# Optimization experiments

Hardware: AMD Instinct MI355X
Metric: run time of the kernel (lower is better)

The kernel has to match this reference:

```python
import jax, jax.numpy as jnp
import numpy as np

HEADS = (4, 2, 1)
OUTS = (32, 16, 2)
NEG_SLOPE = 0.2


def gat_conv(x, src, dst, W, att_s, att_d, b, heads, out_dim, n_nodes, concat):
    # x: [N, Fin] -> h: [N, H, Fout]
    h = (x @ W).reshape(n_nodes, heads, out_dim)
    # per-node attention terms, gathered to edges: [E, H]
    a_src = jnp.sum(h * att_s, axis=-1)
    a_dst = jnp.sum(h * att_d, axis=-1)
    logits = jax.nn.leaky_relu(a_src[src] + a_dst[dst], NEG_SLOPE)
    # segment softmax over incoming edges of each destination node
    lmax = jax.ops.segment_max(logits, dst, num_segments=n_nodes)[dst]
    e = jnp.exp(logits - lmax)
    denom = jax.ops.segment_sum(e, dst, num_segments=n_nodes)[dst]
    alpha = e / denom  # [E, H]
    # weighted message aggregation
    msg = h[src] * alpha[:, :, None]  # [E, H, Fout]
    agg = jax.ops.segment_sum(msg, dst, num_segments=n_nodes)  # [N, H, Fout]
    if concat:
        agg = agg.reshape(n_nodes, heads * out_dim)
    else:
        agg = agg.mean(axis=1)
    return agg + b


def _glorot(key, shape):
    fan = shape[0] + shape[-1] if len(shape) == 2 else shape[-1] * 2
    s = jnp.sqrt(6.0 / fan)
    return jax.random.uniform(key, shape, jnp.float32, -s, s)


def setup_inputs() -> dict:
    key = jax.random.key(0)
    N, E, FIN = 100000, 1600000, 128
    ks = jax.random.split(key, 16)
    x = jax.random.normal(ks[0], (N, FIN), jnp.float32)
    edge_index = jax.random.randint(ks[1], (2, E), 0, N, jnp.int64)
    ins = (FIN, HEADS[0] * OUTS[0], HEADS[1] * OUTS[1])
    d = {"x": x, "edge_index": edge_index}
    for i in range(3):
        H, O = HEADS[i], OUTS[i]
        d[f"W{i+1}"] = _glorot(ks[2 + 4 * i], (ins[i], H * O))
        d[f"att_s{i+1}"] = _glorot(ks[3 + 4 * i], (H, O))
        d[f"att_d{i+1}"] = _glorot(ks[4 + 4 * i], (H, O))
        bdim = H * O if i < 2 else O
        d[f"b{i+1}"] = jnp.zeros((bdim,), jnp.float32)
    return d


def reference(x, edge_index, W1, att_s1, att_d1, b1, W2, att_s2, att_d2, b2, W3, att_s3, att_d3, b3):
    N = x.shape[0]
    loops = jnp.arange(N, dtype=edge_index.dtype)
    src = jnp.concatenate([edge_index[0], loops])
    dst = jnp.concatenate([edge_index[1], loops])
    h = gat_conv(x, src, dst, W1, att_s1, att_d1, b1, HEADS[0], OUTS[0], N, True)
    h = jax.nn.elu(h)
    h = gat_conv(h, src, dst, W2, att_s2, att_d2, b2, HEADS[1], OUTS[1], N, True)
    h = jax.nn.elu(h)
    h = gat_conv(h, src, dst, W3, att_s3, att_d3, b3, HEADS[2], OUTS[2], N, False)
    return jax.nn.log_softmax(h, axis=1)
```

## Files before the change

### kernel.cpp

```cpp
#include <hip/hip_runtime.h>
#include <math.h>

static __device__ __forceinline__ float lrelu(float x){ return fmaxf(x, 0.2f*x); }
static __device__ __forceinline__ float eluf(float x){ return x > 0.f ? x : __expf(x)-1.f; }
static __device__ __forceinline__ float fexp2(float x){ return __builtin_amdgcn_exp2f(x); }
static __device__ __forceinline__ unsigned short f2bf(float f){
  unsigned int u = __float_as_uint(f);
  unsigned int r = (u + 0x7FFFu + ((u>>16)&1u)) >> 16;
  return (unsigned short)r;
}
static __device__ __forceinline__ float bflo(unsigned int u){ return __uint_as_float(u<<16); }
static __device__ __forceinline__ float bfhi(unsigned int u){ return __uint_as_float(u & 0xFFFF0000u); }

#define LOG2E 1.44269504f
#define CLAMP2 115.41f
#define ECAP 4096

typedef __attribute__((ext_vector_type(8))) short short8;
typedef __attribute__((ext_vector_type(4))) float f32x4;

static __device__ __forceinline__ uint4 ld16(const uint4* base, unsigned eoff){
  return *(const uint4*)((const char*)base + (size_t)(eoff*16u));
}
static __device__ __forceinline__ float ldf(const float* base, unsigned eoff){
  return *(const float*)((const char*)base + (size_t)(eoff*4u));
}

#define DETECT_IS64(ei_, s_is64_) \
  if (threadIdx.x < 64){ \
    int w_ = ((const int*)(ei_))[2*threadIdx.x + 1]; \
    unsigned long long b_ = __ballot(w_ != 0); \
    if (threadIdx.x == 0) s_is64_ = (b_ == 0ull); \
  } \
  __syncthreads();

__global__ void k_wprep(const float* __restrict__ W1, const float* __restrict__ W2,
                        unsigned short* __restrict__ wf1, unsigned short* __restrict__ wf2,
                        int* __restrict__ gcnt, int NB){
  int e = blockIdx.x*256 + threadIdx.x;
  if (e < NB) gcnt[e] = 0;
  if (e < 2048){
    int lane = e&63, ct = (e>>6)&7, ks = e>>9;
    int q = lane>>4, n = lane&15;
    union { unsigned short us[8]; uint4 u; } pk;
    #pragma unroll
    for (int j=0;j<8;j++)
      pk.us[j] = f2bf(W1[(ks*32 + q*8 + j)*128 + ct*16 + n]);
    *(uint4*)&wf1[(size_t)e*8] = pk.u;
  } else if (e < 2048+512){
    int e2 = e - 2048;
    int lane = e2&63, ct = (e2>>6)&1, ks = e2>>7;
    int q = lane>>4, n = lane&15;
    union { unsigned short us[8]; uint4 u; } pk;
    #pragma unroll
    for (int j=0;j<8;j++)
      pk.us[j] = f2bf(W2[(ks*32 + q*8 + j)*32 + ct*16 + n]);
    *(uint4*)&wf2[(size_t)e2*8] = pk.u;
  }
}

#define BS_ITEMS 16
__global__ __launch_bounds__(256, 4) void k_scat_gemm1(
    const void* __restrict__ ei, int* __restrict__ gcnt,
    unsigned int* __restrict__ ebuf, int E, int NB, int GS,
    const float* __restrict__ x, const unsigned short* __restrict__ wf,
    const float* __restrict__ atts, const float* __restrict__ attd,
    unsigned short* __restrict__ hb, float* __restrict__ as_, float* __restrict__ ad_,
    int N){
  __shared__ __align__(16) unsigned char smem[32768];
  __shared__ int s_is64;
  int t = threadIdx.x;
  if ((int)blockIdx.x < GS){
    int* lcnt  = (int*)smem;
    int* lbase = lcnt + NB;
    for (int i=t; i<NB; i+=256) lcnt[i]=0;
    DETECT_IS64(ei, s_is64)
    bool is64 = s_is64 != 0;
    int base = blockIdx.x*(256*BS_ITEMS);
    unsigned int ent[BS_ITEMS]; int bk[BS_ITEMS]; int lofs[BS_ITEMS];
    #pragma unroll
    for (int i=0;i<BS_ITEMS;i++){
      int e = base + i*256 + t;
      if (e < E){
        int s, d;
        if (is64){ const long long* p=(const long long*)ei; s=(int)p[e]; d=(int)p[(size_t)E+e]; }
        else     { const int* p=(const int*)ei;            s=p[e];      d=p[(size_t)E+e]; }
        int b = d>>7;
        bk[i] = b;
        ent[i] = (unsigned int)s | ((unsigned int)(d & 127) << 25);
        lofs[i] = atomicAdd(&lcnt[b], 1);
      } else bk[i] = -1;
    }
    __syncthreads();
    for (int i=t; i<NB; i+=256){
      int c = lcnt[i];
      lbase[i] = c ? atomicAdd(&gcnt[i], c) : 0;
    }
    __syncthreads();
    #pragma unroll
    for (int i=0;i<BS_ITEMS;i++){
      if (bk[i] >= 0){
        int pos = lbase[bk[i]] + lofs[i];
        if (pos < ECAP)
          ebuf[(size_t)bk[i]*ECAP + pos] = ent[i];
      }
    }
  } else {
    unsigned short* wsm = (unsigned short*)smem;
    int r0 = ((int)blockIdx.x - GS)*64;
    {
      const uint4* src = (const uint4*)wf;
      uint4* dst = (uint4*)wsm;
      #pragma unroll
      for (int i=0;i<8;i++) dst[t + i*256] = src[t + i*256];
    }
    int w = t>>6, lane = t&63, lm = lane&15, q = lane>>4;
    int rt0 = (w&1)*2;
    int ct0 = (w>>1)*4;
    short8 af[2][4];
    #pragma unroll
    for (int rl=0; rl<2; rl++){
      int gr = r0 + (rt0+rl)*16 + lm;
      bool ok = gr < N;
      const float* xr = &x[(size_t)(ok ? gr : 0)*128];
      #pragma unroll
      for (int ks=0; ks<4; ks++){
        float4 v0 = make_float4(0.f,0.f,0.f,0.f), v1 = v0;
        if (ok){
          v0 = *(const float4*)&xr[ks*32 + q*8];
          v1 = *(const float4*)&xr[ks*32 + q*8 + 4];
        }
        union { unsigned short us[8]; short8 s8; } pk;
        pk.us[0]=f2bf(v0.x); pk.us[1]=f2bf(v0.y); pk.us[2]=f2bf(v0.z); pk.us[3]=f2bf(v0.w);
        pk.us[4]=f2bf(v1.x); pk.us[5]=f2bf(v1.y); pk.us[6]=f2bf(v1.z); pk.us[7]=f2bf(v1.w);
        af[rl][ks] = pk.s8;
      }
    }
    __syncthreads();
    f32x4 acc[2][4];
    #pragma unroll
    for (int a=0;a<2;a++)
      #pragma unroll
      for (int c=0;c<4;c++) acc[a][c] = (f32x4){0.f,0.f,0.f,0.f};
    #pragma unroll
    for (int ks=0;ks<4;ks++){
      #pragma unroll
      for (int c=0;c<4;c++){
        short8 b = *(const short8*)&wsm[((ks*8 + ct0 + c)*64 + lane)*8];
        acc[0][c] = __builtin_amdgcn_mfma_f32_16x16x32_bf16(af[0][ks], b, acc[0][c], 0,0,0);
        acc[1][c] = __builtin_amdgcn_mfma_f32_16x16x32_bf16(af[1][ks], b, acc[1][c], 0,0,0);
      }
    }
    __syncthreads();
    unsigned short* xs = wsm;
    #pragma unroll
    for (int rl=0;rl<2;rl++)
      #pragma unroll
      for (int c=0;c<4;c++)
        #pragma unroll
        for (int r=0;r<4;r++)
          xs[((rt0+rl)*16 + q*4 + r)*136 + (ct0+c)*16 + lm] = f2bf(acc[rl][c][r]);
    __syncthreads();
    {
      #pragma unroll
      for (int i=0;i<4;i++){
        int idx = t + i*256;
        int row = idx>>4, c8 = (idx&15)*8;
        int gr = r0 + row;
        if (gr < N)
          *(uint4*)&hb[(size_t)gr*128 + c8] = *(const uint4*)&xs[row*136 + c8];
      }
    }
    {
      int row = t>>2, h = t&3;
      int gr = r0 + row;
      if (gr < N){
        const unsigned short* hr = &xs[row*136 + h*32];
        const float* sa = atts + h*32;
        const float* da = attd + h*32;
        float ss = 0.f, dd = 0.f;
        #pragma unroll
        for (int o=0;o<32;o+=8){
          uint4 v = *(const uint4*)&hr[o];
          float hv[8] = { bflo(v.x),bfhi(v.x),bflo(v.y),bfhi(v.y),
                          bflo(v.z),bfhi(v.z),bflo(v.w),bfhi(v.w) };
          #pragma unroll
          for (int m=0;m<8;m++){ ss += hv[m]*sa[o+m]; dd += hv[m]*da[o+m]; }
        }
        as_[gr*4+h] = ss*LOG2E; ad_[gr*4+h] = dd*LOG2E;
      }
    }
  }
}

__global__ __launch_bounds__(256) void k_bcsr(const unsigned int* __restrict__ ebuf,
    const int* __restrict__ gcnt,
    int* __restrict__ rp, int* __restrict__ re, int* __restrict__ csr, int N, int NB){
  __shared__ unsigned int lde[ECAP];
  __shared__ unsigned short lofp[ECAP];
  __shared__ int lcnt[128];
  __shared__ int lexc[128];
  __shared__ int sc[256];
  int b = blockIdx.x, t = threadIdx.x;
  int d0 = b<<7;
  int R = N - d0; if (R > 128) R = 128;
  if (t < 128) lcnt[t]=0;
  __syncthreads();
  size_t base = (size_t)b*ECAP;
  int cnt = gcnt[b]; if (cnt > ECAP) cnt = ECAP;
  for (int i=t; i<cnt; i+=256){
    unsigned int e = ebuf[base+i];
    lde[i] = e;
    lofp[i] = (unsigned short)atomicAdd(&lcnt[e>>25], 1);
  }
  __syncthreads();
  int v = (t<128)? lcnt[t] : 0;
  sc[t]=v; __syncthreads();
  for (int off=1; off<128; off<<=1){
    int add = (t>=off)? sc[t-off] : 0;
    __syncthreads();
    sc[t]+=add;
    __syncthreads();
  }
  if (t<128) lexc[t] = sc[t]-v;
  __syncthreads();
  if (t < R){
    int s = (int)base + lexc[t];
    rp[d0+t] = s;
    re[d0+t] = s + lcnt[t];
  }
  for (int i=t; i<cnt; i+=256){
    unsigned int e = lde[i];
    csr[base + lexc[e>>25] + lofp[i]] = (int)(e & 0x1FFFFFFu);
  }
}

__global__ __launch_bounds__(256) void k_mgemm2(const unsigned short* __restrict__ xb,
    const unsigned short* __restrict__ wf,
    const float* __restrict__ atts, const float* __restrict__ attd,
    unsigned short* __restrict__ hb2, float* __restrict__ as_, float* __restrict__ ad_,
    int N){
  __shared__ unsigned short xs[128*136];
  __shared__ unsigned short wsm[512*8];
  int t = threadIdx.x;
  int r0 = blockIdx.x*128;
  {
    #pragma unroll
    for (int i=0;i<2;i++)
      ((uint4*)wsm)[t + i*256] = ((const uint4*)wf)[t + i*256];
  }
  {
    #pragma unroll
    for (int i=0;i<8;i++){
      int idx = t + i*256;
      int row = idx>>4, c8 = (idx&15)*8;
      int gr = r0 + row;
      uint4 v = make_uint4(0u,0u,0u,0u);
      if (gr < N) v = *(const uint4*)&xb[(size_t)gr*128 + c8];
      *(uint4*)&xs[row*136 + c8] = v;
    }
  }
  __syncthreads();
  int w = t>>6, lane = t&63, lm = lane&15, q = lane>>4;
  int rt0 = 2*w;
  f32x4 acc[2][2];
  #pragma unroll
  for (int a=0;a<2;a++){ acc[a][0] = (f32x4){0.f,0.f,0.f,0.f}; acc[a][1] = acc[a][0]; }
  #pragma unroll
  for (int ks=0;ks<4;ks++){
    short8 a0 = *(const short8*)&xs[( rt0   *16 + lm)*136 + ks*32 + q*8];
    short8 a1 = *(const short8*)&xs[((rt0+1)*16 + lm)*136 + ks*32 + q*8];
    #pragma unroll
    for (int c=0;c<2;c++){
      short8 b = *(const short8*)&wsm[((ks*2 + c)*64 + lane)*8];
      acc[0][c] = __builtin_amdgcn_mfma_f32_16x16x32_bf16(a0, b, acc[0][c], 0,0,0);
      acc[1][c] = __builtin_amdgcn_mfma_f32_16x16x32_bf16(a1, b, acc[1][c], 0,0,0);
    }
  }
  __syncthreads();
  #pragma unroll
  for (int rl=0;rl<2;rl++)
    #pragma unroll
    for (int c=0;c<2;c++)
      #pragma unroll
      for (int r=0;r<4;r++)
        xs[((rt0+rl)*16 + q*4 + r)*136 + c*16 + lm] = f2bf(acc[rl][c][r]);
  __syncthreads();
  {
    #pragma unroll
    for (int i=0;i<2;i++){
      int idx = t + i*256;
      int row = idx>>2, c8 = (idx&3)*8;
      int gr = r0 + row;
      if (gr < N)
        *(uint4*)&hb2[(size_t)gr*32 + c8] = *(const uint4*)&xs[row*136 + c8];
    }
  }
  {
    int row = t>>1, h = t&1;
    int gr = r0 + row;
    if (gr < N){
      const unsigned short* hr = &xs[row*136 + h*16];
      const float* sa = atts + h*16;
      const float* da = attd + h*16;
      float ss = 0.f, dd = 0.f;
      #pragma unroll
      for (int o=0;o<16;o+=8){
        uint4 v = *(const uint4*)&hr[o];
        float hv[8] = { bflo(v.x),bfhi(v.x),bflo(v.y),bfhi(v.y),
                        bflo(v.z),bfhi(v.z),bflo(v.w),bfhi(v.w) };
        #pragma unroll
        for (int m=0;m<8;m++){ ss += hv[m]*sa[o+m]; dd += hv[m]*da[o+m]; }
      }
      as_[gr*2+h] = ss*LOG2E; ad_[gr*2+h] = dd*LOG2E;
    }
  }
}

#define ACC8(v_, w_) { \
  a[0]+=w_*bflo(v_.x); a[1]+=w_*bfhi(v_.x); a[2]+=w_*bflo(v_.y); a[3]+=w_*bfhi(v_.y); \
  a[4]+=w_*bflo(v_.z); a[5]+=w_*bfhi(v_.z); a[6]+=w_*bflo(v_.w); a[7]+=w_*bfhi(v_.w); }

__global__ __launch_bounds__(256) void k_agg1(const int* __restrict__ rp, const int* __restrict__ re,
    const int* __restrict__ csr,
    const float* __restrict__ as_, const float* __restrict__ ad_,
    const uint4* __restrict__ hb4, const float* __restrict__ bias,
    unsigned short* __restrict__ outb, int N){
  int n = blockIdx.x*16 + (threadIdx.x>>4);
  if (n >= N) return;
  int li = threadIdx.x & 15, ghead = li>>2;
  int start = rp[n], end = re[n];
  float adh = ldf(ad_, (unsigned)n*4u+ghead);
  float a[8];
  #pragma unroll
  for (int k=0;k<8;k++) a[k]=0.f;
  float wse = fexp2(fminf(lrelu(ldf(as_, (unsigned)n*4u+ghead) + adh), CLAMP2));
  float l = wse;
  { uint4 v = ld16(hb4, (unsigned)n*16u + li); ACC8(v, wse) }
  int i = start;
  for (; i + 1 < end; i += 2){
    int s0 = csr[i];
    int s1 = csr[i+1];
    float w0 = fexp2(fminf(lrelu(ldf(as_, (unsigned)s0*4u+ghead) + adh), CLAMP2));
    float w1 = fexp2(fminf(lrelu(ldf(as_, (unsigned)s1*4u+ghead) + adh), CLAMP2));
    uint4 v0 = ld16(hb4, (unsigned)s0*16u + li);
    uint4 v1 = ld16(hb4, (unsigned)s1*16u + li);
    l += w0 + w1;
    ACC8(v0, w0)
    ACC8(v1, w1)
  }
  if (i < end){
    int s = csr[i];
    float w = fexp2(fminf(lrelu(ldf(as_, (unsigned)s*4u+ghead) + adh), CLAMP2));
    uint4 v = ld16(hb4, (unsigned)s*16u + li);
    l += w;
    ACC8(v, w)
  }
  float invh = 1.f/l;
  float4 b0 = *(const float4*)&bias[li*8];
  float4 b1 = *(const float4*)&bias[li*8+4];
  union { unsigned short us[8]; uint4 v; } pk;
  pk.us[0]=f2bf(eluf(a[0]*invh+b0.x)); pk.us[1]=f2bf(eluf(a[1]*invh+b0.y));
  pk.us[2]=f2bf(eluf(a[2]*invh+b0.z)); pk.us[3]=f2bf(eluf(a[3]*invh+b0.w));
  pk.us[4]=f2bf(eluf(a[4]*invh+b1.x)); pk.us[5]=f2bf(eluf(a[5]*invh+b1.y));
  pk.us[6]=f2bf(eluf(a[6]*invh+b1.z)); pk.us[7]=f2bf(eluf(a[7]*invh+b1.w));
  *(uint4*)&outb[(size_t)n*128 + li*8] = pk.v;
}

__global__ __launch_bounds__(256) void k_agg2(const int* __restrict__ rp, const int* __restrict__ re,
    const int* __restrict__ csr,
    const float* __restrict__ as_, const float* __restrict__ ad_,
    const uint4* __restrict__ hb4, const float* __restrict__ bias,
    const float* __restrict__ W3, const float* __restrict__ atts3,
    const float* __restrict__ attd3,
    float4* __restrict__ pk4, int N){
  int n = blockIdx.x*64 + (threadIdx.x>>2);
  if (n >= N) return;
  int li = threadIdx.x & 3, ghead = li>>1;
  int start = rp[n], end = re[n];
  float adh = ldf(ad_, (unsigned)n*2u+ghead);
  float a[8];
  #pragma unroll
  for (int k=0;k<8;k++) a[k]=0.f;
  float wse = fexp2(fminf(lrelu(ldf(as_, (unsigned)n*2u+ghead) + adh), CLAMP2));
  float l = wse;
  { uint4 v = ld16(hb4, (unsigned)n*4u + li); ACC8(v, wse) }
  int i = start;
  for (; i + 1 < end; i += 2){
    int s0 = csr[i];
    int s1 = csr[i+1];
    float w0 = fexp2(fminf(lrelu(ldf(as_, (unsigned)s0*2u+ghead) + adh), CLAMP2));
    float w1 = fexp2(fminf(lrelu(ldf(as_, (unsigned)s1*2u+ghead) + adh), CLAMP2));
    uint4 v0 = ld16(hb4, (unsigned)s0*4u + li);
    uint4 v1 = ld16(hb4, (unsigned)s1*4u + li);
    l += w0 + w1;
    ACC8(v0, w0)
    ACC8(v1, w1)
  }
  if (i < end){
    int s = csr[i];
    float w = fexp2(fminf(lrelu(ldf(as_, (unsigned)s*2u+ghead) + adh), CLAMP2));
    uint4 v = ld16(hb4, (unsigned)s*4u + li);
    l += w;
    ACC8(v, w)
  }
  float invh = 1.f/l;
  float r0_ = eluf(a[0]*invh + bias[li*8+0]);
  float r1_ = eluf(a[1]*invh + bias[li*8+1]);
  float r2_ = eluf(a[2]*invh + bias[li*8+2]);
  float r3_ = eluf(a[3]*invh + bias[li*8+3]);
  float r4_ = eluf(a[4]*invh + bias[li*8+4]);
  float r5_ = eluf(a[5]*invh + bias[li*8+5]);
  float r6_ = eluf(a[6]*invh + bias[li*8+6]);
  float r7_ = eluf(a[7]*invh + bias[li*8+7]);
  const float* wr = &W3[li*16];
  float p0 = r0_*wr[0] + r1_*wr[2] + r2_*wr[4]  + r3_*wr[6]
           + r4_*wr[8] + r5_*wr[10]+ r6_*wr[12] + r7_*wr[14];
  float p1 = r0_*wr[1] + r1_*wr[3] + r2_*wr[5]  + r3_*wr[7]
           + r4_*wr[9] + r5_*wr[11]+ r6_*wr[13] + r7_*wr[15];
  p0 += __shfl_xor(p0,1); p0 += __shfl_xor(p0,2);
  p1 += __shfl_xor(p1,1); p1 += __shfl_xor(p1,2);
  if (li == 0){
    float4 pk;
    pk.x = p0; pk.y = p1;
    pk.z = (p0*atts3[0] + p1*atts3[1])*LOG2E;
    pk.w = (p0*attd3[0] + p1*attd3[1])*LOG2E;
    pk4[n] = pk;
  }
}

__global__ __launch_bounds__(256) void k_agg3(const int* __restrict__ rp, const int* __restrict__ re,
    const int* __restrict__ csr,
    const float4* __restrict__ pk4, const float* __restrict__ bias,
    float* __restrict__ out, int N){
  int n = blockIdx.x*16 + (threadIdx.x>>4);
  if (n >= N) return;
  int li = threadIdx.x & 15;
  int start = rp[n], end = re[n];
  float4 self = pk4[n];
  float adh = self.w;
  float l = 0.f;
  float2 acc = make_float2(0.f, 0.f);
  for (int i=start+li; i<end; i+=16){
    int s = csr[i];
    float4 ps = pk4[s];
    float w = fexp2(fminf(lrelu(ps.z + adh), CLAMP2));
    l += w;
    acc.x += w*ps.x; acc.y += w*ps.y;
  }
  if (li == 0){
    float w = fexp2(fminf(lrelu(self.z + adh), CLAMP2));
    l += w;
    acc.x += w*self.x; acc.y += w*self.y;
  }
  #pragma unroll
  for (int msk=1; msk<16; msk<<=1){
    l += __shfl_xor(l, msk);
    acc.x += __shfl_xor(acc.x, msk);
    acc.y += __shfl_xor(acc.y, msk);
  }
  if (li == 0){
    float inv = 1.f/l;
    float g0 = acc.x*inv + bias[0];
    float g1 = acc.y*inv + bias[1];
    float mm = fmaxf(g0, g1);
    float lse = mm + logf(__expf(g0-mm) + __expf(g1-mm));
    *(float2*)&out[2*n] = make_float2(g0-lse, g1-lse);
  }
}

extern "C" void kernel_launch(void* const* d_in, const int* in_sizes, int n_in,
                              void* d_out, int out_size, void* d_ws, size_t ws_size,
                              hipStream_t stream) {
  const float* x   = (const float*)d_in[0];
  const void*  ei  = d_in[1];
  const float* W1  = (const float*)d_in[2];
  const float* as1 = (const float*)d_in[3];
  const float* ad1 = (const float*)d_in[4];
  const float* b1  = (const float*)d_in[5];
  const float* W2  = (const float*)d_in[6];
  const float* as2 = (const float*)d_in[7];
  const float* ad2 = (const float*)d_in[8];
  const float* b2  = (const float*)d_in[9];
  const float* W3  = (const float*)d_in[10];
  const float* as3 = (const float*)d_in[11];
  const float* ad3 = (const float*)d_in[12];
  const float* b3  = (const float*)d_in[13];

  int N = in_sizes[0] / 128;
  int E = in_sizes[1] / 2;
  int NB = (N + 127) >> 7;

  char* w = (char*)d_ws;
  size_t off = 0;
  auto alloc = [&](size_t bytes)->void*{
    void* p = w + off; off += (bytes + 255) & ~(size_t)255; return p;
  };
  int*   gcnt    = (int*)alloc((size_t)NB*4);
  int*   rp      = (int*)alloc((size_t)N*4);
  int*   re      = (int*)alloc((size_t)N*4);
  unsigned int* ebuf = (unsigned int*)alloc((size_t)NB*ECAP*4);
  int*   csr     = (int*)alloc((size_t)NB*ECAP*4);
  float* as_buf  = (float*)alloc((size_t)N*4*4);
  float* ad_buf  = (float*)alloc((size_t)N*4*4);
  unsigned short* wf1 = (unsigned short*)alloc(2048*8*2);
  unsigned short* wf2 = (unsigned short*)alloc(512*8*2);
  unsigned short* hb  = (unsigned short*)alloc((size_t)N*128*2);
  unsigned short* xb  = (unsigned short*)alloc((size_t)N*128*2);
  unsigned short* hb2 = (unsigned short*)alloc((size_t)N*32*2);
  float4* pk4    = (float4*)alloc((size_t)N*16);
  if (off > ws_size) return;

  k_wprep<<<10, 256, 0, stream>>>(W1, W2, wf1, wf2, gcnt, NB);

  int GS = (E + 256*BS_ITEMS - 1) / (256*BS_ITEMS);
  int G1 = (N + 63)/64;
  k_scat_gemm1<<<GS + G1, 256, 0, stream>>>(ei, gcnt, ebuf, E, NB, GS,
                                            x, wf1, as1, ad1, hb, as_buf, ad_buf, N);
  k_bcsr<<<NB, 256, 0, stream>>>(ebuf, gcnt, rp, re, csr, N, NB);

  k_agg1<<<(N + 15)/16, 256, 0, stream>>>(rp, re, csr, as_buf, ad_buf, (const uint4*)hb, b1, xb, N);

  k_mgemm2<<<(N + 127)/128, 256, 0, stream>>>(xb, wf2, as2, ad2, hb2, as_buf, ad_buf, N);
  k_agg2<<<(N + 63)/64, 256, 0, stream>>>(rp, re, csr, as_buf, ad_buf, (const uint4*)hb2, b2,
                                          W3, as3, ad3, pk4, N);

  k_agg3<<<(N + 15)/16, 256, 0, stream>>>(rp, re, csr, pk4, b3, (float*)d_out, N);
}
```

Before: 290.1 us.

## Sort bucket entries in shared memory before scatter; split agg1 into launches

The edge bucketing phase now computes a block-local prefix sum over bucket counts, stages entries sorted by bucket in shared memory, and then writes each bucket's run contiguously to the global edge buffer. This replaces scattered per-entry global writes with contiguous runs. The layer-1 aggregation kernel is also split into four sequential launches over node ranges, likely to improve cache locality of gathered features. The costs are extra syncs, a serial per-bucket copy loop and extra launch overhead.

Result: slower. 316.2 us (+9.0%).

```diff
diff --git a/kernel.cpp b/kernel.cpp
--- a/kernel.cpp
+++ b/kernel.cpp
@@ -72,7 +72,10 @@
   int t = threadIdx.x;
   if ((int)blockIdx.x < GS){
     int* lcnt  = (int*)smem;
-    int* lbase = lcnt + NB;
+    int* lpre  = lcnt + NB;
+    int* gbse  = lpre + NB;
+    int* csum  = gbse + NB;
+    unsigned int* sorted = (unsigned int*)(csum + 256);
     for (int i=t; i<NB; i+=256) lcnt[i]=0;
     DETECT_IS64(ei, s_is64)
     bool is64 = s_is64 != 0;
@@ -92,17 +95,40 @@
       } else bk[i] = -1;
     }
     __syncthreads();
+    int c0 = t*4, s = 0;
+    #pragma unroll
+    for (int k=0;k<4;k++){ int idx=c0+k; if (idx<NB) s += lcnt[idx]; }
+    csum[t] = s;
     for (int i=t; i<NB; i+=256){
       int c = lcnt[i];
-      lbase[i] = c ? atomicAdd(&gcnt[i], c) : 0;
-    }
-    __syncthreads();
-    #pragma unroll
-    for (int i=0;i<BS_ITEMS;i++){
-      if (bk[i] >= 0){
-        int pos = lbase[bk[i]] + lofs[i];
-        if (pos < ECAP)
-          ebuf[(size_t)bk[i]*ECAP + pos] = ent[i];
+      gbse[i] = c ? atomicAdd(&gcnt[i], c) : 0;
+    }
+    __syncthreads();
+    for (int off=1; off<256; off<<=1){
+      int add = (t>=off)? csum[t-off] : 0;
+      __syncthreads();
+      csum[t] += add;
+      __syncthreads();
+    }
+    int run = (t==0) ? 0 : csum[t-1];
+    #pragma unroll
+    for (int k=0;k<4;k++){
+      int idx = c0+k;
+      if (idx<NB){ lpre[idx] = run; run += lcnt[idx]; }
+    }
+    __syncthreads();
+    #pragma unroll
+    for (int i=0;i<BS_ITEMS;i++)
+      if (bk[i] >= 0) sorted[lpre[bk[i]] + lofs[i]] = ent[i];
+    __syncthreads();
+    for (int b=t; b<NB; b+=256){
+      int c = lcnt[b];
+      if (!c) continue;
+      int p = lpre[b], g = gbse[b];
+      unsigned int* dst = &ebuf[(size_t)b*ECAP];
+      for (int k=0;k<c;k++){
+        int pos = g+k;
+        if (pos < ECAP) dst[pos] = sorted[p+k];
       }
     }
   } else {
@@ -325,9 +351,9 @@
     const int* __restrict__ csr,
     const float* __restrict__ as_, const float* __restrict__ ad_,
     const uint4* __restrict__ hb4, const float* __restrict__ bias,
-    unsigned short* __restrict__ outb, int N){
-  int n = blockIdx.x*16 + (threadIdx.x>>4);
-  if (n >= N) return;
+    unsigned short* __restrict__ outb, int n0, int nlim){
+  int n = n0 + blockIdx.x*16 + (threadIdx.x>>4);
+  if (n >= nlim) return;
   int li = threadIdx.x & 15, ghead = li>>2;
   int start = rp[n], end = re[n];
   float adh = ldf(ad_, (unsigned)n*4u+ghead);
@@ -519,7 +545,14 @@
                                             x, wf1, as1, ad1, hb, as_buf, ad_buf, N);
   k_bcsr<<<NB, 256, 0, stream>>>(ebuf, gcnt, rp, re, csr, N, NB);
 
-  k_agg1<<<(N + 15)/16, 256, 0, stream>>>(rp, re, csr, as_buf, ad_buf, (const uint4*)hb, b1, xb, N);
+  {
+    int step = (((N + 3) / 4) + 15) & ~15;
+    for (int n0 = 0; n0 < N; n0 += step){
+      int nl = N - n0 < step ? N : n0 + step;
+      k_agg1<<<(nl - n0 + 15)/16, 256, 0, stream>>>(rp, re, csr, as_buf, ad_buf,
+                                                    (const uint4*)hb, b1, xb, n0, nl);
+    }
+  }
 
   k_mgemm2<<<(N + 127)/128, 256, 0, stream>>>(xb, wf2, as2, ad2, hb2, as_buf, ad_buf, N);
   k_agg2<<<(N + 63)/64, 256, 0, stream>>>(rp, re, csr, as_buf, ad_buf, (const uint4*)hb2, b2,
```
